# Performance work log

Measured on AMD Instinct MI355X. Metric: run time of the kernel, lower is better.

Reference implementation:

```python
import jax, jax.numpy as jnp
import numpy as np

L, B, T, D, H, F, V = 8, 2, 1024, 1024, 16, 4096, 50257


def _ln(x, w, b):
    m = jnp.mean(x, axis=-1, keepdims=True)
    v = jnp.mean((x - m) ** 2, axis=-1, keepdims=True)
    return (x - m) * jax.lax.rsqrt(v + 1e-5) * w + b


def setup_inputs() -> dict:
    key = jax.random.key(0)
    ks = iter(jax.random.split(key, 16))
    s = jnp.float32(0.02)
    w = lambda shape: jax.random.normal(next(ks), shape, jnp.float32) * s
    return {
        'idx': jax.random.randint(next(ks), (B, T), 0, V, jnp.int32),
        'emb': w((V, D)),
        'pos_emb': w((T, D)),
        'ln1_w': jnp.ones((L, D), jnp.float32),
        'ln1_b': jnp.zeros((L, D), jnp.float32),
        'qkv_w': w((L, D, 3 * D)),
        'qkv_b': jnp.zeros((L, 3 * D), jnp.float32),
        'ln2_w': jnp.ones((L, D), jnp.float32),
        'ln2_b': jnp.zeros((L, D), jnp.float32),
        'fc1_w': w((L, D, F)),
        'fc1_b': jnp.zeros((L, F), jnp.float32),
        'fc2_w': w((L, F, D)),
        'fc2_b': jnp.zeros((L, D), jnp.float32),
        'lnf_w': jnp.ones((D,), jnp.float32),
        'lnf_b': jnp.zeros((D,), jnp.float32),
        'head_w': w((D, V)),
        'head_b': jnp.zeros((V,), jnp.float32),
    }


def reference(idx, emb, pos_emb, ln1_w, ln1_b, qkv_w, qkv_b, ln2_w, ln2_b,
              fc1_w, fc1_b, fc2_w, fc2_b, lnf_w, lnf_b, head_w, head_b):
    b, t = idx.shape
    d = emb.shape[1]
    hd = d // H
    x = emb[idx] + pos_emb[:t]                      # [b,t,d]
    mask = jnp.tril(jnp.ones((t, t), bool))         # causal mask
    inv_scale = jnp.float32(1.0 / (d ** 0.5))       # NOTE: source scales by sqrt(full dim), not head_dim

    def layer(x, p):
        l1w, l1b, qw, qb, l2w, l2b, f1w, f1b, f2w, f2b = p
        h = _ln(x, l1w, l1b)
        qkv = h @ qw + qb                           # [b,t,3d]
        q, k, v = jnp.split(qkv, 3, axis=-1)
        q = q.reshape(b, t, H, hd)
        k = k.reshape(b, t, H, hd)
        v = v.reshape(b, t, H, hd)
        logits = jnp.einsum('bqhe,bkhe->bhqk', q, k) * inv_scale
        logits = jnp.where(mask, logits, -jnp.inf)
        attn = jax.nn.softmax(logits, axis=-1)
        o = jnp.einsum('bhqk,bkhe->bqhe', attn, v).reshape(b, t, d)
        x = x + o                                   # no output projection in source
        h = _ln(x, l2w, l2b)
        h = jax.nn.gelu(h @ f1w + f1b, approximate=False)
        h = jax.nn.gelu(h @ f2w + f2b, approximate=False)  # GELU after fc2 too, per source
        return x + h, None

    x, _ = jax.lax.scan(
        layer, x,
        (ln1_w, ln1_b, qkv_w, qkv_b, ln2_w, ln2_b, fc1_w, fc1_b, fc2_w, fc2_b))
    x = _ln(x, lnf_w, lnf_b)
    return x @ head_w + head_b                      # [b,t,V] logits
```

## Files before the change

kernel.cpp:

```cpp
#include <hip/hip_runtime.h>
#include <math.h>

#define Ln 8
#define Bn 2
#define Tn 1024
#define Dm 1024
#define Hn 16
#define Fm 4096
#define Vn 50257
#define NTOK 2048

typedef unsigned short u16;
typedef u16   u16x8  __attribute__((ext_vector_type(8)));
typedef __bf16 bf16x8 __attribute__((ext_vector_type(8)));
typedef float f32x4  __attribute__((ext_vector_type(4)));

__device__ __forceinline__ u16 f2bf(float f){
  unsigned u = __builtin_bit_cast(unsigned, f);
  u += 0x7FFFu + ((u >> 16) & 1u);
  return (u16)(u >> 16);
}
__device__ __forceinline__ float bf2f(u16 s){
  return __builtin_bit_cast(float, ((unsigned)s) << 16);
}
__device__ __forceinline__ float gelu_f(float v){
  return 0.5f * v * (1.0f + erff(v * 0.70710678118654752440f));
}
__device__ __forceinline__ void gload16(const void* g, void* l){
  __builtin_amdgcn_global_load_lds(
      (const __attribute__((address_space(1))) void*)g,
      (__attribute__((address_space(3))) void*)l, 16, 0, 0);
}

__global__ __launch_bounds__(256) void embed_kernel(const int* __restrict__ idx,
                                                    const float* __restrict__ emb,
                                                    const float* __restrict__ pos,
                                                    float* __restrict__ x){
  int row = blockIdx.x;
  int t = row & (Tn - 1);
  int id = idx[row];
  const float4* e = (const float4*)(emb + (size_t)id * Dm);
  const float4* p = (const float4*)(pos + (size_t)t * Dm);
  float4* o = (float4*)(x + (size_t)row * Dm);
  int i = threadIdx.x;
  float4 a = e[i], b = p[i];
  o[i] = make_float4(a.x + b.x, a.y + b.y, a.z + b.z, a.w + b.w);
}

__global__ __launch_bounds__(256) void ln_kernel(const float* __restrict__ xin,
                                                 const float* __restrict__ w,
                                                 const float* __restrict__ bb,
                                                 u16* __restrict__ out){
  int row = blockIdx.x;
  int t = threadIdx.x;
  float4 v = ((const float4*)(xin + (size_t)row * Dm))[t];
  float s  = v.x + v.y + v.z + v.w;
  float s2 = v.x*v.x + v.y*v.y + v.z*v.z + v.w*v.w;
  #pragma unroll
  for (int off = 1; off < 64; off <<= 1){
    s  += __shfl_xor(s, off);
    s2 += __shfl_xor(s2, off);
  }
  __shared__ float red[8];
  int wv = t >> 6, lane = t & 63;
  if (lane == 0){ red[wv] = s; red[4 + wv] = s2; }
  __syncthreads();
  s  = red[0] + red[1] + red[2] + red[3];
  s2 = red[4] + red[5] + red[6] + red[7];
  float mean = s * (1.0f / Dm);
  float var  = s2 * (1.0f / Dm) - mean * mean;
  float rs = rsqrtf(var + 1e-5f);
  float4 wv4 = ((const float4*)w)[t];
  float4 bv4 = ((const float4*)bb)[t];
  u16 o4[4];
  o4[0] = f2bf((v.x - mean) * rs * wv4.x + bv4.x);
  o4[1] = f2bf((v.y - mean) * rs * wv4.y + bv4.y);
  o4[2] = f2bf((v.z - mean) * rs * wv4.z + bv4.z);
  o4[3] = f2bf((v.w - mean) * rs * wv4.w + bv4.w);
  *(uint2*)(out + (size_t)row * Dm + t * 4) = *(uint2*)o4;
}

__device__ __forceinline__ void trans_tile(const float* __restrict__ src,
                                           u16* __restrict__ dst,
                                           int N, int K, int srcCol, int dstRow, int k0){
  __shared__ float tile[64][66];
  int t = threadIdx.x;
  int rr = t >> 4, nc = (t & 15) * 4;
  #pragma unroll
  for (int u = 0; u < 4; u++){
    int kk = rr + u * 16;
    int gn = srcCol + nc;
    const float* sp = src + (size_t)(k0 + kk) * N;
    float4 v;
    if (gn + 3 < N) v = *(const float4*)(sp + gn);
    else {
      v.x = (gn     < N) ? sp[gn]     : 0.0f;
      v.y = (gn + 1 < N) ? sp[gn + 1] : 0.0f;
      v.z = (gn + 2 < N) ? sp[gn + 2] : 0.0f;
      v.w = (gn + 3 < N) ? sp[gn + 3] : 0.0f;
    }
    tile[kk][nc]     = v.x;
    tile[kk][nc + 1] = v.y;
    tile[kk][nc + 2] = v.z;
    tile[kk][nc + 3] = v.w;
  }
  __syncthreads();
  int np = t >> 2, c = t & 3;
  u16* dp = dst + (size_t)(dstRow + np) * K + k0;
  u16 pk[8];
  #pragma unroll
  for (int j = 0; j < 8; j++) pk[j] = f2bf(tile[c*8 + j][np]);
  *(int4*)(dp + c*8) = *(int4*)pk;
  #pragma unroll
  for (int j = 0; j < 8; j++) pk[j] = f2bf(tile[32 + c*8 + j][np]);
  *(int4*)(dp + 32 + c*8) = *(int4*)pk;
}

__global__ __launch_bounds__(256) void transpose_w(const float* __restrict__ Bw,
                                                   u16* __restrict__ Bt,
                                                   int N, int K, int c0){
  int n0 = blockIdx.x * 64, k0 = blockIdx.y * 64;
  trans_tile(Bw, Bt, N, K, c0 + n0, n0, k0);
}

__global__ __launch_bounds__(256) void mega_transpose(const float* __restrict__ qkvw,
                                                      const float* __restrict__ fc1w,
                                                      const float* __restrict__ fc2w,
                                                      const float* __restrict__ headw,
                                                      u16* __restrict__ Wq,
                                                      u16* __restrict__ W1,
                                                      u16* __restrict__ W2,
                                                      u16* __restrict__ Wh){
  int id = blockIdx.x;
  const float* src; u16* dst; int N, K, n0, k0;
  if (id < 6144){
    int l = id / 768, r = id % 768;
    n0 = (r % 48) * 64; k0 = (r / 48) * 64;
    src = qkvw + (size_t)l * Dm * 3072; dst = Wq + (size_t)l * 3072 * Dm;
    N = 3072; K = Dm;
  } else if (id < 14336){
    int id2 = id - 6144;
    int l = id2 / 1024, r = id2 % 1024;
    n0 = (r % 64) * 64; k0 = (r / 64) * 64;
    src = fc1w + (size_t)l * Dm * Fm; dst = W1 + (size_t)l * Fm * Dm;
    N = Fm; K = Dm;
  } else if (id < 22528){
    int id2 = id - 14336;
    int l = id2 / 1024, r = id2 % 1024;
    n0 = (r % 16) * 64; k0 = (r / 16) * 64;
    src = fc2w + (size_t)l * Fm * Dm; dst = W2 + (size_t)l * Dm * Fm;
    N = Dm; K = Fm;
  } else {
    int id2 = id - 22528;
    n0 = (id2 % 788) * 64; k0 = (id2 / 788) * 64;
    src = headw; dst = Wh;
    N = Vn; K = Dm;
  }
  trans_tile(src, dst, N, K, n0, n0, k0);
}

template<int MODE, int BMt, int BNt, int WM, int WN, bool SWZ>
__global__ __launch_bounds__(256) void gemm_kernel(const u16* __restrict__ A,
                                                   const u16* __restrict__ Bt,
                                                   const float* __restrict__ bias,
                                                   void* __restrict__ outp,
                                                   float* __restrict__ resid,
                                                   u16* __restrict__ vT,
                                                   int K, int Nout, int c0){
  constexpr int MR = BMt / (WM * 16);
  constexpr int NR = BNt / (WN * 16);
  __shared__ u16 sA[BMt][64];
  __shared__ u16 sB[BNt][64];
  int t = threadIdx.x;
  int lane = t & 63, w = t >> 6;
  int wm = w / WN, wn = w % WN;
  int lr = lane & 15, lg = lane >> 4;
  int m0, n0;
  if (SWZ){
    int orig = blockIdx.x;
    int q = gridDim.x >> 3;
    int wg = (orig & 7) * q + (orig >> 3);
    m0 = (wg & 15) * BMt;
    n0 = (wg >> 4) * BNt;
  } else {
    m0 = blockIdx.y * BMt; n0 = blockIdx.x * BNt;
  }

  f32x4 acc[MR][NR] = {};

  int srow = lane >> 3;
  int gcs = ((lane & 7) ^ (lane >> 3)) * 8;
  int cswz = (lr & 7) << 3;

  for (int k0 = 0; k0 < K; k0 += 64){
    __syncthreads();
    #pragma unroll
    for (int i = 0; i < BMt/32; i++){
      int rbase = i*32 + w*8;
      gload16(A + (size_t)(m0 + rbase + srow) * K + k0 + gcs, (char*)&sA[rbase][0]);
    }
    #pragma unroll
    for (int i = 0; i < BNt/32; i++){
      int rbase = i*32 + w*8;
      gload16(Bt + (size_t)(n0 + rbase + srow) * K + k0 + gcs, (char*)&sB[rbase][0]);
    }
    __syncthreads();
    #pragma unroll
    for (int kk = 0; kk < 2; kk++){
      bf16x8 af[MR], bfr[NR];
      #pragma unroll
      for (int i = 0; i < MR; i++) af[i]  = *(const bf16x8*)&sA[wm*(MR*16) + i*16 + lr][(kk*32 + lg*8) ^ cswz];
      #pragma unroll
      for (int j = 0; j < NR; j++) bfr[j] = *(const bf16x8*)&sB[wn*(NR*16) + j*16 + lr][(kk*32 + lg*8) ^ cswz];
      #pragma unroll
      for (int i = 0; i < MR; i++)
        #pragma unroll
        for (int j = 0; j < NR; j++)
          acc[i][j] = __builtin_amdgcn_mfma_f32_16x16x32_bf16(af[i], bfr[j], acc[i][j], 0, 0, 0);
    }
  }

  #pragma unroll
  for (int i = 0; i < MR; i++){
    int gr0 = m0 + wm*(MR*16) + i*16 + lg*4;
    #pragma unroll
    for (int j = 0; j < NR; j++){
      int gc = c0 + n0 + wn*(NR*16) + j*16 + lr;
      if (MODE == 3 && gc >= Nout) continue;
      float bb = bias[gc];
      if (MODE == 0 && gc >= 2048){
        int hh = (gc - 2048) >> 6, dd = (gc - 2048) & 63;
        int b_ = gr0 >> 10, tt = gr0 & 1023;
        u16 pk[4];
        #pragma unroll
        for (int r = 0; r < 4; r++) pk[r] = f2bf(acc[i][j][r] + bb);
        *(uint2*)&vT[((size_t)((b_*Hn + hh)*64 + dd))*Tn + tt] = *(uint2*)pk;
        continue;
      }
      #pragma unroll
      for (int r = 0; r < 4; r++){
        float v = acc[i][j][r] + bb;
        size_t oi = (size_t)(gr0 + r) * Nout + gc;
        if (MODE == 0)      ((u16*)outp)[oi] = f2bf(v);
        else if (MODE == 1) ((u16*)outp)[oi] = f2bf(gelu_f(v));
        else if (MODE == 2) resid[oi] = resid[oi] + gelu_f(v);
        else                ((float*)outp)[oi] = v;
      }
    }
  }
}

#define BARR() __builtin_amdgcn_s_barrier()
#define LGK0() asm volatile("s_waitcnt lgkmcnt(0)" ::: "memory")
#define VMC4() asm volatile("s_waitcnt vmcnt(4)" ::: "memory")

__global__ __launch_bounds__(512) void head_gemm_8ph(const u16* __restrict__ A,
                                                     const u16* __restrict__ Bw,
                                                     const float* __restrict__ bias,
                                                     float* __restrict__ out){
  __shared__ u16 sA[2][256][64];
  __shared__ u16 sB[2][256][64];
  int t = threadIdx.x, lane = t & 63, w = t >> 6;
  int wm = w >> 2, wn = w & 3;
  int lr = lane & 15, lg = lane >> 4;
  int orig = blockIdx.x;
  int wg = (orig & 7) * (gridDim.x >> 3) + (orig >> 3);
  int m0g = (wg & 7) << 8;
  int n0g = (wg >> 3) << 8;

  int srow = w*8 + (lane >> 3);
  int scol = ((lane & 7) ^ (lane >> 3)) * 8;
  const u16* Abase = A  + (size_t)(m0g + srow) * 1024 + scol;
  const u16* Bbase = Bw + (size_t)(n0g + srow) * 1024 + scol;

  f32x4 acc[8][4] = {};
  bf16x8 a[4][2], b0[2][2], b1[2][2];
  int rsw = (lr & 7) << 3;

  auto stA = [&](int buf, int half, int tile){
    const u16* s = Abase + (size_t)half*128*1024 + tile*64;
    gload16(s,           &sA[buf][half*128 +      w*8][0]);
    gload16(s + 64*1024, &sA[buf][half*128 + 64 + w*8][0]);
  };
  auto stB = [&](int buf, int half, int tile){
    const u16* s = Bbase + (size_t)half*128*1024 + tile*64;
    gload16(s,           &sB[buf][half*128 +      w*8][0]);
    gload16(s + 64*1024, &sB[buf][half*128 + 64 + w*8][0]);
  };
  auto rdA = [&](int buf, int half){
    #pragma unroll
    for (int i = 0; i < 4; i++)
      #pragma unroll
      for (int kk = 0; kk < 2; kk++)
        a[i][kk] = *(const bf16x8*)&sA[buf][wm*128 + half*64 + i*16 + lr][(kk*32 + lg*8) ^ rsw];
  };
  auto rdB = [&](int buf, int half, bf16x8 (&bb)[2][2]){
    #pragma unroll
    for (int j = 0; j < 2; j++)
      #pragma unroll
      for (int kk = 0; kk < 2; kk++)
        bb[j][kk] = *(const bf16x8*)&sB[buf][wn*64 + half*32 + j*16 + lr][(kk*32 + lg*8) ^ rsw];
  };
  auto MF = [&](int mb, int nb, bf16x8 (&bb)[2][2]){
    __builtin_amdgcn_s_setprio(1);
    #pragma unroll
    for (int kk = 0; kk < 2; kk++)
      #pragma unroll
      for (int i = 0; i < 4; i++)
        #pragma unroll
        for (int j = 0; j < 2; j++)
          acc[mb+i][nb+j] = __builtin_amdgcn_mfma_f32_16x16x32_bf16(a[i][kk], bb[j][kk], acc[mb+i][nb+j], 0, 0, 0);
    __builtin_amdgcn_s_setprio(0);
  };

  stA(0,0,0); stA(0,1,0); stB(0,0,0); stB(0,1,0);
  stB(1,0,1); stB(1,1,1);
  VMC4();
  BARR();

  for (int it = 0; it < 8; ++it){
    int T = it * 2;
    rdA(0,0); rdB(0,0,b0);
    stA(1,0,T+1);
    BARR(); LGK0(); MF(0,0,b0); BARR();
    rdB(0,1,b1);
    stA(1,1,T+1);
    BARR(); LGK0(); MF(0,2,b1); BARR();
    rdA(0,1);
    if (T+2 < 16) stB(0,0,T+2);
    BARR(); LGK0(); MF(4,2,b1); BARR();
    if (T+2 < 16) stB(0,1,T+2);
    BARR(); MF(4,0,b0); VMC4(); BARR();
    rdA(1,0); rdB(1,0,b0);
    if (T+2 < 16) stA(0,0,T+2);
    BARR(); LGK0(); MF(0,0,b0); BARR();
    rdB(1,1,b1);
    if (T+2 < 16) stA(0,1,T+2);
    BARR(); LGK0(); MF(0,2,b1); BARR();
    rdA(1,1);
    if (T+3 < 16) stB(1,0,T+3);
    BARR(); LGK0(); MF(4,2,b1); BARR();
    if (T+3 < 16) stB(1,1,T+3);
    BARR(); MF(4,0,b0); VMC4(); BARR();
  }

  #pragma unroll
  for (int m = 0; m < 8; m++){
    int gr = m0g + wm*128 + m*16 + lg*4;
    #pragma unroll
    for (int n = 0; n < 4; n++){
      int gc = n0g + wn*64 + n*16 + lr;
      if (gc < Vn){
        float bb = bias[gc];
        #pragma unroll
        for (int r = 0; r < 4; r++)
          out[(size_t)(gr + r) * Vn + gc] = acc[m][n][r] + bb;
      }
    }
  }
}

__global__ __launch_bounds__(256) void attn_mfma(const u16* __restrict__ qkv,
                                                 const u16* __restrict__ vT,
                                                 float* __restrict__ x){
  int bid = blockIdx.x;
  int bh = bid & 31;
  int j = bid >> 5;
  int qt = (j < 8) ? (15 - j) : (j - 8);
  int b = bh >> 4, h_ = bh & 15;
  int t = threadIdx.x;
  int w = t >> 6, lane = t & 63;
  int lr = lane & 15, lg = lane >> 4;

  __shared__ u16 sK [2][64][72];
  __shared__ u16 sVt[2][64][72];
  __shared__ u16 sP [64][72];

  const u16* qbase = qkv + ((size_t)(b*Tn + qt*64 + w*16 + lr)) * 3*Dm + h_*64 + lg*8;
  bf16x8 qf[2];
  #pragma unroll
  for (int i = 0; i < 2; i++){
    u16x8 raw = *(const u16x8*)(qbase + i * 32);
    #pragma unroll
    for (int u = 0; u < 8; u++) qf[i][u] = (__bf16)(bf2f(raw[u]) * 0.03125f);
  }

  f32x4 o_[4] = {};
  float m_[4], l_[4];
  #pragma unroll
  for (int r = 0; r < 4; r++){ m_[r] = -INFINITY; l_[r] = 0.0f; }

  int sr = t >> 2, scc = (t & 3) * 16;
  const u16* kbase = qkv + ((size_t)(b*Tn + sr)) * 3*Dm + Dm + h_*64 + scc;
  const u16* vbase = vT + ((size_t)(bh*64 + sr)) * Tn + scc;
  int4 kr0, kr1, vr0, vr1;

  kr0 = *(const int4*)(kbase);     kr1 = *(const int4*)(kbase + 8);
  vr0 = *(const int4*)(vbase);     vr1 = *(const int4*)(vbase + 8);
  *(int4*)&sK [0][sr][scc]     = kr0;  *(int4*)&sK [0][sr][scc + 8] = kr1;
  *(int4*)&sVt[0][sr][scc]     = vr0;  *(int4*)&sVt[0][sr][scc + 8] = vr1;

  for (int kt = 0; kt <= qt; kt++){
    int cur = kt & 1;
    if (kt < qt){
      const u16* kb = kbase + (size_t)(kt + 1) * 64 * 3 * Dm;
      const u16* vb = vbase + (kt + 1) * 64;
      kr0 = *(const int4*)(kb);    kr1 = *(const int4*)(kb + 8);
      vr0 = *(const int4*)(vb);    vr1 = *(const int4*)(vb + 8);
    }
    __syncthreads();

    f32x4 s[4] = {};
    __builtin_amdgcn_s_setprio(1);
    #pragma unroll
    for (int kf = 0; kf < 2; kf++){
      #pragma unroll
      for (int nf = 0; nf < 4; nf++){
        bf16x8 kfrag = *(const bf16x8*)&sK[cur][nf*16 + lr][kf*32 + lg*8];
        s[nf] = __builtin_amdgcn_mfma_f32_16x16x32_bf16(qf[kf], kfrag, s[nf], 0, 0, 0);
      }
    }
    __builtin_amdgcn_s_setprio(0);

    bool lastt = (kt == qt);
    float tmax[4] = {-INFINITY, -INFINITY, -INFINITY, -INFINITY};
    #pragma unroll
    for (int nf = 0; nf < 4; nf++)
      #pragma unroll
      for (int r = 0; r < 4; r++){
        float v = s[nf][r];
        if (lastt){
          int kkg = nf*16 + lr, qg = w*16 + lg*4 + r;
          if (kkg > qg) v = -INFINITY;
        }
        s[nf][r] = v;
        tmax[r] = fmaxf(tmax[r], v);
      }
    #pragma unroll
    for (int r = 0; r < 4; r++){
      tmax[r] = fmaxf(tmax[r], __shfl_xor(tmax[r], 1));
      tmax[r] = fmaxf(tmax[r], __shfl_xor(tmax[r], 2));
      tmax[r] = fmaxf(tmax[r], __shfl_xor(tmax[r], 4));
      tmax[r] = fmaxf(tmax[r], __shfl_xor(tmax[r], 8));
    }
    float resc[4], psum[4];
    #pragma unroll
    for (int r = 0; r < 4; r++){
      float nm = fmaxf(m_[r], tmax[r]);
      resc[r] = __expf(m_[r] - nm);
      m_[r] = nm;
      psum[r] = 0.0f;
    }
    #pragma unroll
    for (int nf = 0; nf < 4; nf++)
      #pragma unroll
      for (int r = 0; r < 4; r++){
        float pv = __expf(s[nf][r] - m_[r]);
        s[nf][r] = pv;
        psum[r] += pv;
      }
    #pragma unroll
    for (int r = 0; r < 4; r++){
      psum[r] += __shfl_xor(psum[r], 1);
      psum[r] += __shfl_xor(psum[r], 2);
      psum[r] += __shfl_xor(psum[r], 4);
      psum[r] += __shfl_xor(psum[r], 8);
      l_[r] = l_[r] * resc[r] + psum[r];
    }
    #pragma unroll
    for (int df = 0; df < 4; df++)
      #pragma unroll
      for (int r = 0; r < 4; r++)
        o_[df][r] *= resc[r];

    #pragma unroll
    for (int nf = 0; nf < 4; nf++)
      #pragma unroll
      for (int r = 0; r < 4; r++)
        sP[w*16 + lg*4 + r][nf*16 + lr] = f2bf(s[nf][r]);

    __builtin_amdgcn_s_setprio(1);
    #pragma unroll
    for (int kf = 0; kf < 2; kf++){
      bf16x8 pfrag = *(const bf16x8*)&sP[w*16 + lr][kf*32 + lg*8];
      #pragma unroll
      for (int df = 0; df < 4; df++){
        bf16x8 vfrag = *(const bf16x8*)&sVt[cur][df*16 + lr][kf*32 + lg*8];
        o_[df] = __builtin_amdgcn_mfma_f32_16x16x32_bf16(pfrag, vfrag, o_[df], 0, 0, 0);
      }
    }
    __builtin_amdgcn_s_setprio(0);

    if (kt < qt){
      int nxt = cur ^ 1;
      *(int4*)&sK [nxt][sr][scc]     = kr0;  *(int4*)&sK [nxt][sr][scc + 8] = kr1;
      *(int4*)&sVt[nxt][sr][scc]     = vr0;  *(int4*)&sVt[nxt][sr][scc + 8] = vr1;
    }
  }

  float inv[4];
  #pragma unroll
  for (int r = 0; r < 4; r++) inv[r] = 1.0f / l_[r];
  #pragma unroll
  for (int df = 0; df < 4; df++)
    #pragma unroll
    for (int r = 0; r < 4; r++){
      float* xr = x + ((size_t)(b*Tn + qt*64 + w*16 + lg*4 + r)) * Dm + h_*64 + df*16 + lr;
      *xr += o_[df][r] * inv[r];
    }
}

extern "C" void kernel_launch(void* const* d_in, const int* in_sizes, int n_in,
                              void* d_out, int out_size, void* d_ws, size_t ws_size,
                              hipStream_t stream){
  const int*   idx   = (const int*)  d_in[0];
  const float* emb   = (const float*)d_in[1];
  const float* pos   = (const float*)d_in[2];
  const float* ln1w  = (const float*)d_in[3];
  const float* ln1b  = (const float*)d_in[4];
  const float* qkvw  = (const float*)d_in[5];
  const float* qkvb  = (const float*)d_in[6];
  const float* ln2w  = (const float*)d_in[7];
  const float* ln2b  = (const float*)d_in[8];
  const float* fc1w  = (const float*)d_in[9];
  const float* fc1b  = (const float*)d_in[10];
  const float* fc2w  = (const float*)d_in[11];
  const float* fc2b  = (const float*)d_in[12];
  const float* lnfw  = (const float*)d_in[13];
  const float* lnfb  = (const float*)d_in[14];
  const float* headw = (const float*)d_in[15];
  const float* headb = (const float*)d_in[16];
  float* out = (float*)d_out;

  const size_t MB = 1u << 20;
  char* ws = (char*)d_ws;
  float* x   = (float*)(ws);
  u16*   h   = (u16*)  (ws + 8*MB);
  u16*   qkv = (u16*)  (ws + 12*MB);
  u16*   f1  = (u16*)  (ws + 24*MB);

  bool mega    = ws_size >= 320*MB;
  bool bighead = ws_size >= 116*MB;

  u16 *vT, *Bt = nullptr, *BtF = nullptr, *Wq = nullptr, *W1 = nullptr, *W2 = nullptr, *Wh = nullptr;
  if (mega){
    vT = (u16*)(ws + 40*MB);
    Wq = (u16*)(ws + 44*MB);
    W1 = (u16*)(ws + 92*MB);
    W2 = (u16*)(ws + 156*MB);
    Wh = (u16*)(ws + 220*MB);
  } else {
    Bt  = (u16*)(ws + 40*MB);
    vT  = (u16*)(ws + 48*MB);
    BtF = (u16*)(ws + 12*MB);
  }

  if (mega)
    mega_transpose<<<35136, 256, 0, stream>>>(qkvw, fc1w, fc2w, headw, Wq, W1, W2, Wh);

  embed_kernel<<<NTOK, 256, 0, stream>>>(idx, emb, pos, x);

  for (int l = 0; l < Ln; l++){
    const u16* Bq = mega ? Wq + (size_t)l*3072*Dm : Bt;
    const u16* B1 = mega ? W1 + (size_t)l*Fm*Dm   : Bt;
    const u16* B2 = mega ? W2 + (size_t)l*Dm*Fm   : Bt;
    ln_kernel<<<NTOK, 256, 0, stream>>>(x, ln1w + l*Dm, ln1b + l*Dm, h);
    if (!mega) transpose_w<<<dim3(3072/64, Dm/64), 256, 0, stream>>>(qkvw + (size_t)l*Dm*3072, Bt, 3072, Dm, 0);
    gemm_kernel<0, 64,128,1,4,false><<<dim3(3072/128, NTOK/64), 256, 0, stream>>>(h, Bq, qkvb + l*3072, qkv, nullptr, vT, Dm, 3072, 0);
    attn_mfma<<<512, 256, 0, stream>>>(qkv, vT, x);
    ln_kernel<<<NTOK, 256, 0, stream>>>(x, ln2w + l*Dm, ln2b + l*Dm, h);
    if (!mega) transpose_w<<<dim3(Fm/64, Dm/64), 256, 0, stream>>>(fc1w + (size_t)l*Dm*Fm, Bt, Fm, Dm, 0);
    gemm_kernel<1,128,128,2,2,false><<<dim3(Fm/128, NTOK/128), 256, 0, stream>>>(h, B1, fc1b + l*Fm, f1, nullptr, nullptr, Dm, Fm, 0);
    if (!mega) transpose_w<<<dim3(Dm/64, Fm/64), 256, 0, stream>>>(fc2w + (size_t)l*Fm*Dm, Bt, Dm, Fm, 0);
    gemm_kernel<2, 64,128,1,4,false><<<dim3(Dm/128, NTOK/64), 256, 0, stream>>>(f1, B2, fc2b + l*Dm, nullptr, x, nullptr, Fm, Dm, 0);
  }

  ln_kernel<<<NTOK, 256, 0, stream>>>(x, lnfw, lnfb, h);

  if (mega){
    head_gemm_8ph<<<1576, 512, 0, stream>>>(h, Wh, headb, out);
  } else if (bighead){
    transpose_w<<<dim3(786, Dm/64), 256, 0, stream>>>(headw, BtF, Vn, Dm, 0);
    gemm_kernel<3,128,128,2,2,true><<<6288, 256, 0, stream>>>(h, BtF, headb, out, nullptr, nullptr, Dm, Vn, 0);
  } else {
    const int CHUNK = 4096;
    for (int c0 = 0; c0 < Vn; c0 += CHUNK){
      int W = Vn - c0; if (W > CHUNK) W = CHUNK;
      int ngx = (W + 127) / 128;
      transpose_w<<<dim3(ngx * 2, Dm/64), 256, 0, stream>>>(headw, Bt, Vn, Dm, c0);
      gemm_kernel<3,128,128,2,2,false><<<dim3(ngx, NTOK/128), 256, 0, stream>>>(h, Bt, headb, out, nullptr, nullptr, Dm, Vn, c0);
    }
  }
}
```

Baseline: 1.885 ms.

## Make head GEMM persistent per vocab column strip with overlapped epilogue stores

```diff
diff --git a/kernel.cpp b/kernel.cpp
--- a/kernel.cpp
+++ b/kernel.cpp
@@ -252,38 +252,42 @@
 
 #define BARR() __builtin_amdgcn_s_barrier()
 #define LGK0() asm volatile("s_waitcnt lgkmcnt(0)" ::: "memory")
-#define VMC4() asm volatile("s_waitcnt vmcnt(4)" ::: "memory")
-
-__global__ __launch_bounds__(512) void head_gemm_8ph(const u16* __restrict__ A,
-                                                     const u16* __restrict__ Bw,
-                                                     const float* __restrict__ bias,
-                                                     float* __restrict__ out){
+#define VMC(n) asm volatile("s_waitcnt vmcnt(" #n ")" ::: "memory")
+
+__global__ __launch_bounds__(512) void head_gemm_pers(const u16* __restrict__ A,
+                                                      const u16* __restrict__ Bw,
+                                                      const float* __restrict__ bias,
+                                                      float* __restrict__ out){
   __shared__ u16 sA[2][256][64];
   __shared__ u16 sB[2][256][64];
   int t = threadIdx.x, lane = t & 63, w = t >> 6;
   int wm = w >> 2, wn = w & 3;
   int lr = lane & 15, lg = lane >> 4;
-  int orig = blockIdx.x;
-  int wg = (orig & 7) * (gridDim.x >> 3) + (orig >> 3);
-  int m0g = (wg & 7) << 8;
-  int n0g = (wg >> 3) << 8;
+  int n0g = blockIdx.x << 8;
 
   int srow = w*8 + (lane >> 3);
   int scol = ((lane & 7) ^ (lane >> 3)) * 8;
-  const u16* Abase = A  + (size_t)(m0g + srow) * 1024 + scol;
   const u16* Bbase = Bw + (size_t)(n0g + srow) * 1024 + scol;
+
+  float bcol[4];
+  #pragma unroll
+  for (int c = 0; c < 4; c++){
+    int gc = n0g + wn*64 + c*16 + lr;
+    bcol[c] = (gc < Vn) ? bias[gc] : 0.0f;
+  }
 
   f32x4 acc[8][4] = {};
   bf16x8 a[4][2], b0[2][2], b1[2][2];
   int rsw = (lr & 7) << 3;
 
-  auto stA = [&](int buf, int half, int tile){
-    const u16* s = Abase + (size_t)half*128*1024 + tile*64;
+  auto abase = [&](int m){ return A + (size_t)((m << 8) + srow) * 1024 + scol; };
+  auto stA = [&](int buf, int half, const u16* base, int kt){
+    const u16* s = base + (size_t)half*128*1024 + kt*64;
     gload16(s,           &sA[buf][half*128 +      w*8][0]);
     gload16(s + 64*1024, &sA[buf][half*128 + 64 + w*8][0]);
   };
-  auto stB = [&](int buf, int half, int tile){
-    const u16* s = Bbase + (size_t)half*128*1024 + tile*64;
+  auto stB = [&](int buf, int half, int kt){
+    const u16* s = Bbase + (size_t)half*128*1024 + (kt & 15)*64;
     gload16(s,           &sB[buf][half*128 +      w*8][0]);
     gload16(s + 64*1024, &sB[buf][half*128 + 64 + w*8][0]);
   };
@@ -301,63 +305,111 @@
       for (int kk = 0; kk < 2; kk++)
         bb[j][kk] = *(const bf16x8*)&sB[buf][wn*64 + half*32 + j*16 + lr][(kk*32 + lg*8) ^ rsw];
   };
-  auto MF = [&](int mb, int nb, bf16x8 (&bb)[2][2]){
+  auto MF = [&](int mb, int nb, bf16x8 (&bb)[2][2], bool zc){
     __builtin_amdgcn_s_setprio(1);
     #pragma unroll
     for (int kk = 0; kk < 2; kk++)
       #pragma unroll
       for (int i = 0; i < 4; i++)
         #pragma unroll
-        for (int j = 0; j < 2; j++)
-          acc[mb+i][nb+j] = __builtin_amdgcn_mfma_f32_16x16x32_bf16(a[i][kk], bb[j][kk], acc[mb+i][nb+j], 0, 0, 0);
+        for (int j = 0; j < 2; j++){
+          f32x4 c = (zc && kk == 0) ? (f32x4){0.f,0.f,0.f,0.f} : acc[mb+i][nb+j];
+          acc[mb+i][nb+j] = __builtin_amdgcn_mfma_f32_16x16x32_bf16(a[i][kk], bb[j][kk], c, 0, 0, 0);
+        }
     __builtin_amdgcn_s_setprio(0);
   };
-
-  stA(0,0,0); stA(0,1,0); stB(0,0,0); stB(0,1,0);
-  stB(1,0,1); stB(1,1,1);
-  VMC4();
-  BARR();
-
-  for (int it = 0; it < 8; ++it){
-    int T = it * 2;
-    rdA(0,0); rdB(0,0,b0);
-    stA(1,0,T+1);
-    BARR(); LGK0(); MF(0,0,b0); BARR();
-    rdB(0,1,b1);
-    stA(1,1,T+1);
-    BARR(); LGK0(); MF(0,2,b1); BARR();
-    rdA(0,1);
-    if (T+2 < 16) stB(0,0,T+2);
-    BARR(); LGK0(); MF(4,2,b1); BARR();
-    if (T+2 < 16) stB(0,1,T+2);
-    BARR(); MF(4,0,b0); VMC4(); BARR();
-    rdA(1,0); rdB(1,0,b0);
-    if (T+2 < 16) stA(0,0,T+2);
-    BARR(); LGK0(); MF(0,0,b0); BARR();
-    rdB(1,1,b1);
-    if (T+2 < 16) stA(0,1,T+2);
-    BARR(); LGK0(); MF(0,2,b1); BARR();
-    rdA(1,1);
-    if (T+3 < 16) stB(1,0,T+3);
-    BARR(); LGK0(); MF(4,2,b1); BARR();
-    if (T+3 < 16) stB(1,1,T+3);
-    BARR(); MF(4,0,b0); VMC4(); BARR();
-  }
-
-  #pragma unroll
-  for (int m = 0; m < 8; m++){
-    int gr = m0g + wm*128 + m*16 + lg*4;
-    #pragma unroll
-    for (int n = 0; n < 4; n++){
-      int gc = n0g + wn*64 + n*16 + lr;
+  auto storeS = [&](int mo, int q, int s){
+    const int mbq[4] = {0,0,4,4}, nbq[4] = {0,2,2,0};
+    int mb = mbq[q], nb = nbq[q];
+    #pragma unroll
+    for (int j = 0; j < 2; j++){
+      int row = (mo << 8) + wm*128 + (mb + s)*16 + lg*4;
+      int cs = nb + j;
+      int gc = n0g + wn*64 + cs*16 + lr;
       if (gc < Vn){
-        float bb = bias[gc];
+        float bbv = bcol[cs];
         #pragma unroll
         for (int r = 0; r < 4; r++)
-          out[(size_t)(gr + r) * Vn + gc] = acc[m][n][r] + bb;
+          out[(size_t)(row + r) * Vn + gc] = acc[mb + s][nb + j][r] + bbv;
       }
     }
-  }
+  };
+
+  const u16* Acur = abase(0);
+  stA(0,0,Acur,0); stA(0,1,Acur,0); stB(0,0,0); stB(0,1,0); stB(1,0,1); stB(1,1,1);
+  VMC(4);
+  BARR();
+
+  for (int m = 0; m < 8; m++){
+    const u16* Anxt = abase((m + 1) & 7);
+    bool ho = (m > 0);
+    int mo = m - 1;
+    rdA(0,0); rdB(0,0,b0); stA(1,0,Acur,1);
+    if (ho){ storeS(mo,0,3); storeS(mo,1,2); storeS(mo,2,1); storeS(mo,3,0); }
+    BARR(); LGK0(); MF(0,0,b0,true); BARR();
+    rdB(0,1,b1); stA(1,1,Acur,1);
+    if (ho){ storeS(mo,1,3); storeS(mo,2,2); storeS(mo,3,1); }
+    BARR(); LGK0(); MF(0,2,b1,true); BARR();
+    rdA(0,1); stB(0,0,2);
+    if (ho){ storeS(mo,2,3); storeS(mo,3,2); }
+    BARR(); LGK0(); MF(4,2,b1,true); BARR();
+    stB(0,1,2);
+    if (ho){ storeS(mo,3,3); }
+    BARR(); MF(4,0,b0,true);
+    if (ho) VMC(44); else VMC(4);
+    BARR();
+    rdA(1,0); rdB(1,0,b0); stA(0,0,Acur,2);
+    BARR(); LGK0(); MF(0,0,b0,false); BARR();
+    rdB(1,1,b1); stA(0,1,Acur,2);
+    BARR(); LGK0(); MF(0,2,b1,false); BARR();
+    rdA(1,1); stB(1,0,3);
+    BARR(); LGK0(); MF(4,2,b1,false); BARR();
+    stB(1,1,3);
+    BARR(); MF(4,0,b0,false); VMC(4); BARR();
+    for (int it = 1; it < 7; ++it){
+      int T = it * 2;
+      rdA(0,0); rdB(0,0,b0); stA(1,0,Acur,T+1);
+      BARR(); LGK0(); MF(0,0,b0,false); BARR();
+      rdB(0,1,b1); stA(1,1,Acur,T+1);
+      BARR(); LGK0(); MF(0,2,b1,false); BARR();
+      rdA(0,1); stB(0,0,T+2);
+      BARR(); LGK0(); MF(4,2,b1,false); BARR();
+      stB(0,1,T+2);
+      BARR(); MF(4,0,b0,false); VMC(4); BARR();
+      rdA(1,0); rdB(1,0,b0); stA(0,0,Acur,T+2);
+      BARR(); LGK0(); MF(0,0,b0,false); BARR();
+      rdB(1,1,b1); stA(0,1,Acur,T+2);
+      BARR(); LGK0(); MF(0,2,b1,false); BARR();
+      rdA(1,1); stB(1,0,T+3);
+      BARR(); LGK0(); MF(4,2,b1,false); BARR();
+      stB(1,1,T+3);
+      BARR(); MF(4,0,b0,false); VMC(4); BARR();
+    }
+    rdA(0,0); rdB(0,0,b0); stA(1,0,Acur,15);
+    BARR(); LGK0(); MF(0,0,b0,false); BARR();
+    rdB(0,1,b1); stA(1,1,Acur,15);
+    BARR(); LGK0(); MF(0,2,b1,false); BARR();
+    rdA(0,1); stB(0,0,16);
+    BARR(); LGK0(); MF(4,2,b1,false); BARR();
+    stB(0,1,16);
+    BARR(); MF(4,0,b0,false); VMC(4); BARR();
+    rdA(1,0); rdB(1,0,b0); stA(0,0,Anxt,0);
+    BARR(); LGK0(); MF(0,0,b0,false); BARR();
+    rdB(1,1,b1); stA(0,1,Anxt,0);
+    storeS(m,0,0);
+    BARR(); LGK0(); MF(0,2,b1,false); BARR();
+    rdA(1,1); stB(1,0,17);
+    storeS(m,0,1); storeS(m,1,0);
+    BARR(); LGK0(); MF(4,2,b1,false); BARR();
+    stB(1,1,17);
+    storeS(m,0,2); storeS(m,1,1); storeS(m,2,0);
+    BARR(); MF(4,0,b0,false); VMC(44); BARR();
+    Acur = Anxt;
+  }
+  storeS(7,0,3);
+  storeS(7,1,2); storeS(7,1,3);
+  storeS(7,2,1); storeS(7,2,2); storeS(7,2,3);
+  storeS(7,3,0); storeS(7,3,1); storeS(7,3,2); storeS(7,3,3);
 }
 
 __global__ __launch_bounds__(256) void attn_mfma(const u16* __restrict__ qkv,
@@ -578,7 +630,7 @@
   ln_kernel<<<NTOK, 256, 0, stream>>>(x, lnfw, lnfb, h);
 
   if (mega){
-    head_gemm_8ph<<<1576, 512, 0, stream>>>(h, Wh, headb, out);
+    head_gemm_pers<<<197, 512, 0, stream>>>(h, Wh, headb, out);
   } else if (bighead){
     transpose_w<<<dim3(786, Dm/64), 256, 0, stream>>>(headw, BtF, Vn, Dm, 0);
     gemm_kernel<3,128,128,2,2,true><<<6288, 256, 0, stream>>>(h, BtF, headb, out, nullptr, nullptr, Dm, Vn, 0);
```

New measurement: 1.956 ms. 1.04x slower.
